# Kernel tuning notes

Hardware: AMD Instinct MI355X
Metric: run time of the kernel (lower is better)

The kernel has to match this reference:

```python
import jax, jax.numpy as jnp
import numpy as np

D_MODEL = 1024
D_FF = 4096
LN_EPS = 1e-5


def _layer_norm(x, gamma, beta):
    mu = jnp.mean(x, axis=-1, keepdims=True)
    var = jnp.mean(jnp.square(x - mu), axis=-1, keepdims=True)
    return (x - mu) * jax.lax.rsqrt(var + LN_EPS) * gamma + beta


def setup_inputs() -> dict:
    key = jax.random.key(0)
    ks = jax.random.split(key, 16)
    B, S, D, F = 2, 2048, D_MODEL, D_FF
    s_d = 1.0 / np.sqrt(D)
    s_f = 1.0 / np.sqrt(F)
    u = lambda k, shape, s: jax.random.uniform(k, shape, jnp.float32, -s, s)
    return {
        "x": jax.random.normal(ks[0], (B, S, D), jnp.float32),
        "wq": u(ks[1], (D, D), s_d), "bq": u(ks[2], (D,), s_d),
        "wk": u(ks[3], (D, D), s_d), "bk": u(ks[4], (D,), s_d),
        "wv": u(ks[5], (D, D), s_d), "bv": u(ks[6], (D,), s_d),
        "wo": u(ks[7], (D, D), s_d), "bo": u(ks[8], (D,), s_d),
        "w1": u(ks[9], (F, D), s_d), "b1": u(ks[10], (F,), s_d),
        "w2": u(ks[11], (D, F), s_f), "b2": u(ks[12], (D,), s_f),
        "g1": jnp.ones((D,), jnp.float32), "be1": jnp.zeros((D,), jnp.float32),
        "g2": jnp.ones((D,), jnp.float32), "be2": jnp.zeros((D,), jnp.float32),
        "num_heads": 16,
    }


def reference(x, wq, bq, wk, bk, wv, bv, wo, bo, w1, b1, w2, b2, g1, be1, g2, be2, num_heads):
    B, S, D = x.shape
    H = num_heads
    dk = D // H
    scale = 1.0 / np.sqrt(dk)

    # --- self-attention (pre-norm) ---
    h = _layer_norm(x, g1, be1)
    q = (h @ wq.T + bq).reshape(B, S, H, dk)
    k = (h @ wk.T + bk).reshape(B, S, H, dk)
    v = (h @ wv.T + bv).reshape(B, S, H, dk)
    scores = jnp.einsum("bqhd,bkhd->bhqk", q, k) * scale  # [B,H,S,S]
    attn = jax.nn.softmax(scores, axis=-1)
    ctx = jnp.einsum("bhqk,bkhd->bqhd", attn, v).reshape(B, S, D)
    x = x + ctx @ wo.T + bo

    # --- feed-forward (pre-norm, exact GELU as in torch default) ---
    h = _layer_norm(x, g2, be2)
    h = jax.nn.gelu(h @ w1.T + b1, approximate=False)
    x = x + h @ w2.T + b2
    return x
```

## Files before the change

### kernel.cpp

```cpp
#include <hip/hip_runtime.h>

typedef __attribute__((ext_vector_type(8))) __bf16 bf16x8;
typedef __attribute__((ext_vector_type(4))) __bf16 bf16x4;
typedef __attribute__((ext_vector_type(4))) float floatx4;
typedef void __attribute__((address_space(3))) lds_void_t;
typedef const void __attribute__((address_space(1))) gbl_void_t;

#define D_MODEL 1024
#define SEQ     2048
#define BATCH   2
#define NH      16
#define DK      64
#define DFF     4096
#define NTOK    (BATCH * SEQ)
#define QKVS    3072

#if __has_builtin(__builtin_amdgcn_exp2f)
#define EXP2(x) __builtin_amdgcn_exp2f(x)
#else
#define EXP2(x) exp2f(x)
#endif

__device__ __forceinline__ float gelu_exact(float x) {
    return 0.5f * x * (1.0f + erff(x * 0.70710678118654752f));
}

__global__ __launch_bounds__(256) void cast_all(const float* __restrict__ wq,
                                                const float* __restrict__ wk,
                                                const float* __restrict__ wv,
                                                const float* __restrict__ wo,
                                                const float* __restrict__ w1,
                                                const float* __restrict__ w2,
                                                __bf16* __restrict__ wqkvB,
                                                __bf16* __restrict__ woB,
                                                __bf16* __restrict__ w1B,
                                                __bf16* __restrict__ w2B) {
    int blk = blockIdx.x;
    const float* src;
    __bf16* dst;
    int base;
    const int NDD8 = (D_MODEL * D_MODEL) / 2048;
    if (blk < NDD8)          { src = wq; dst = wqkvB;                     base = blk; }
    else if (blk < 2 * NDD8) { src = wk; dst = wqkvB + D_MODEL * D_MODEL; base = blk - NDD8; }
    else if (blk < 3 * NDD8) { src = wv; dst = wqkvB + 2 * D_MODEL * D_MODEL; base = blk - 2 * NDD8; }
    else if (blk < 4 * NDD8) { src = wo; dst = woB;                       base = blk - 3 * NDD8; }
    else if (blk < 8 * NDD8) { src = w1; dst = w1B;                       base = blk - 4 * NDD8; }
    else                     { src = w2; dst = w2B;                       base = blk - 8 * NDD8; }
    int i = (base * 256 + threadIdx.x) * 8;
    floatx4 a = *(const floatx4*)(src + i);
    floatx4 b = *(const floatx4*)(src + i + 4);
    bf16x8 o;
    for (int j = 0; j < 4; ++j) { o[j] = (__bf16)a[j]; o[4 + j] = (__bf16)b[j]; }
    *(bf16x8*)(dst + i) = o;
}

__global__ __launch_bounds__(64) void ln_kernel(const float* __restrict__ x,
                                                const float* __restrict__ g,
                                                const float* __restrict__ b,
                                                __bf16* __restrict__ out) {
    int row = blockIdx.x, lane = threadIdx.x, base = lane * 16;
    const float* xr = x + (size_t)row * D_MODEL + base;
    float v[16];
    for (int j = 0; j < 4; ++j) {
        floatx4 a = *(const floatx4*)(xr + 4 * j);
        for (int i = 0; i < 4; ++i) v[4 * j + i] = a[i];
    }
    float s = 0.f, sq = 0.f;
    for (int i = 0; i < 16; ++i) { s += v[i]; sq += v[i] * v[i]; }
    for (int o = 1; o < 64; o <<= 1) { s += __shfl_xor(s, o); sq += __shfl_xor(sq, o); }
    float mu = s * (1.0f / D_MODEL);
    float var = sq * (1.0f / D_MODEL) - mu * mu;
    float rstd = rsqrtf(fmaxf(var, 0.f) + 1e-5f);

    const floatx4* gp = (const floatx4*)(g + base);
    const floatx4* bp = (const floatx4*)(b + base);
    bf16x8 o0, o1;
    for (int j = 0; j < 2; ++j) {
        floatx4 gv0 = gp[2 * j], gv1 = gp[2 * j + 1];
        floatx4 bv0 = bp[2 * j], bv1 = bp[2 * j + 1];
        for (int i = 0; i < 4; ++i) {
            float r0 = (v[8 * j + i] - mu) * rstd * gv0[i] + bv0[i];
            float r1 = (v[8 * j + 4 + i] - mu) * rstd * gv1[i] + bv1[i];
            if (j == 0) { o0[i] = (__bf16)r0; o0[4 + i] = (__bf16)r1; }
            else        { o1[i] = (__bf16)r0; o1[4 + i] = (__bf16)r1; }
        }
    }
    bf16x8* op = (bf16x8*)(out + (size_t)row * D_MODEL + base);
    op[0] = o0; op[1] = o1;
}

__global__ __launch_bounds__(64) void reduce_ln(const float* __restrict__ p0,
                                                const float* __restrict__ p1,
                                                const float* __restrict__ res,
                                                const float* __restrict__ bias,
                                                const float* __restrict__ g,
                                                const float* __restrict__ be,
                                                float* __restrict__ x1,
                                                __bf16* __restrict__ h2) {
    int row = blockIdx.x, lane = threadIdx.x, base = lane * 16;
    size_t off = (size_t)row * D_MODEL + base;
    float v[16];
    for (int j = 0; j < 4; ++j) {
        floatx4 a = *(const floatx4*)(p0 + off + 4 * j);
        floatx4 b = *(const floatx4*)(p1 + off + 4 * j);
        floatx4 r = *(const floatx4*)(res + off + 4 * j);
        floatx4 bv = *(const floatx4*)(bias + base + 4 * j);
        floatx4 o;
        for (int i = 0; i < 4; ++i) { o[i] = a[i] + b[i] + r[i] + bv[i]; v[4 * j + i] = o[i]; }
        *(floatx4*)(x1 + off + 4 * j) = o;
    }
    float s = 0.f, sq = 0.f;
    for (int i = 0; i < 16; ++i) { s += v[i]; sq += v[i] * v[i]; }
    for (int o = 1; o < 64; o <<= 1) { s += __shfl_xor(s, o); sq += __shfl_xor(sq, o); }
    float mu = s * (1.0f / D_MODEL);
    float var = sq * (1.0f / D_MODEL) - mu * mu;
    float rstd = rsqrtf(fmaxf(var, 0.f) + 1e-5f);

    const floatx4* gp = (const floatx4*)(g + base);
    const floatx4* bp = (const floatx4*)(be + base);
    bf16x8 o0, o1;
    for (int j = 0; j < 2; ++j) {
        floatx4 gv0 = gp[2 * j], gv1 = gp[2 * j + 1];
        floatx4 bv0 = bp[2 * j], bv1 = bp[2 * j + 1];
        for (int i = 0; i < 4; ++i) {
            float r0 = (v[8 * j + i] - mu) * rstd * gv0[i] + bv0[i];
            float r1 = (v[8 * j + 4 + i] - mu) * rstd * gv1[i] + bv1[i];
            if (j == 0) { o0[i] = (__bf16)r0; o0[4 + i] = (__bf16)r1; }
            else        { o1[i] = (__bf16)r0; o1[4 + i] = (__bf16)r1; }
        }
    }
    bf16x8* op = (bf16x8*)(h2 + off);
    op[0] = o0; op[1] = o1;
}

template <typename OutT, bool GELU, bool TRIBIAS, int KSPLIT>
__global__ __launch_bounds__(256) void gemm_bt(const __bf16* __restrict__ A,
                                               const __bf16* __restrict__ W,
                                               const float* __restrict__ bias0,
                                               const float* __restrict__ bias1,
                                               const float* __restrict__ bias2,
                                               const float* __restrict__ res,
                                               OutT* out, float* part1,
                                               int M, int N, int K) {
    __shared__ __bf16 AsF[2][4096];
    __shared__ __bf16 WsF[2][4096];

    int m0 = blockIdx.y * 128, n0 = blockIdx.x * 128;
    int t = threadIdx.x;
    int lane = t & 63, wave = t >> 6;
    int wm = (wave >> 1) * 64, wn = (wave & 1) * 64;
    int fr = lane & 15, quad = lane >> 4;
    int scol = quad * 8;

    int Ks = K / KSPLIT;
    int kbeg = (KSPLIT > 1) ? blockIdx.z * Ks : 0;

    floatx4 acc[4][4] = {};

    const __bf16* Abase = A + kbeg;
    const __bf16* Wbase = W + kbeg;

    auto stage = [&](int buf, int k0) {
#pragma unroll
        for (int p = 0; p < 2; ++p) {
            int blk = p * 4 + wave;
            int row = (blk >> 2) * 64 + (blk & 3) * 16 + fr;
            __builtin_amdgcn_global_load_lds(
                (gbl_void_t*)(Abase + (size_t)(m0 + row) * K + k0 + scol),
                (lds_void_t*)&AsF[buf][blk * 512], 16, 0, 0);
            __builtin_amdgcn_global_load_lds(
                (gbl_void_t*)(Wbase + (size_t)(n0 + row) * K + k0 + scol),
                (lds_void_t*)&WsF[buf][blk * 512], 16, 0, 0);
        }
    };

    auto compute = [&](int buf) {
        bf16x8 af[4], wf[4];
#pragma unroll
        for (int i = 0; i < 4; ++i)
            af[i] = *(const bf16x8*)&AsF[buf][((wave >> 1) * 4 + i) * 512 + lane * 8];
#pragma unroll
        for (int i = 0; i < 4; ++i)
            wf[i] = *(const bf16x8*)&WsF[buf][((wave & 1) * 4 + i) * 512 + lane * 8];
#pragma unroll
        for (int mi = 0; mi < 4; ++mi)
#pragma unroll
            for (int ni = 0; ni < 4; ++ni)
                acc[mi][ni] = __builtin_amdgcn_mfma_f32_16x16x32_bf16(wf[ni], af[mi], acc[mi][ni], 0, 0, 0);
    };

    int nsteps = Ks / 32;
    stage(0, 0);
    for (int s = 0; s < nsteps; ++s) {
        int cur = s & 1;
        __syncthreads();
        if (s + 1 < nsteps) stage(cur ^ 1, (s + 1) * 32);
        compute(cur);
    }

    if (KSPLIT > 1) {
        float* pb = (blockIdx.z == 0) ? (float*)out : part1;
#pragma unroll
        for (int mi = 0; mi < 4; ++mi) {
            int row = m0 + wm + mi * 16 + fr;
#pragma unroll
            for (int ni = 0; ni < 4; ++ni) {
                int col = n0 + wn + ni * 16 + quad * 4;
                *(floatx4*)(pb + (size_t)row * N + col) = acc[mi][ni];
            }
        }
    } else {
#pragma unroll
        for (int mi = 0; mi < 4; ++mi) {
            int row = m0 + wm + mi * 16 + fr;
#pragma unroll
            for (int ni = 0; ni < 4; ++ni) {
                int col = n0 + wn + ni * 16 + quad * 4;
                const float* bp = bias0;
                int bcol = col;
                if (TRIBIAS) { bp = col < 1024 ? bias0 : (col < 2048 ? bias1 : bias2); bcol = col & 1023; }
                floatx4 bv4 = *(const floatx4*)(bp + bcol);
                floatx4 v;
#pragma unroll
                for (int r = 0; r < 4; ++r) {
                    float x = acc[mi][ni][r] + bv4[r];
                    if (GELU) x = gelu_exact(x);
                    v[r] = x;
                }
                if (res) {
                    floatx4 r4 = *(const floatx4*)(res + (size_t)row * N + col);
#pragma unroll
                    for (int r = 0; r < 4; ++r) v[r] += r4[r];
                }
                if constexpr (sizeof(OutT) == 2) {
                    bf16x4 pk;
#pragma unroll
                    for (int r = 0; r < 4; ++r) pk[r] = (__bf16)v[r];
                    *(bf16x4*)((__bf16*)out + (size_t)row * N + col) = pk;
                } else {
                    *(floatx4*)((float*)out + (size_t)row * N + col) = v;
                }
            }
        }
    }
}

template <typename OutT, bool GELU, bool TRIBIAS>
__global__ __launch_bounds__(512) void gemm256(const __bf16* __restrict__ A,
                                               const __bf16* __restrict__ W,
                                               const float* __restrict__ bias0,
                                               const float* __restrict__ bias1,
                                               const float* __restrict__ bias2,
                                               OutT* out,
                                               int M, int N, int K) {
    __shared__ __bf16 AsF[2][8192];
    __shared__ __bf16 WsF[2][4096];

    int m0 = blockIdx.y * 256, n0 = blockIdx.x * 128;
    int t = threadIdx.x;
    int lane = t & 63, wave = t >> 6;
    int wm = (wave >> 1) * 64, wn = (wave & 1) * 64;
    int fr = lane & 15, quad = lane >> 4;
    int scol = quad * 8;

    floatx4 acc[4][4] = {};

    auto stage = [&](int buf, int k0) {
#pragma unroll
        for (int p = 0; p < 3; ++p) {
            int blk = wave * 3 + p;
            if (blk < 16) {
                int row = blk * 16 + fr;
                __builtin_amdgcn_global_load_lds(
                    (gbl_void_t*)(A + (size_t)(m0 + row) * K + k0 + scol),
                    (lds_void_t*)&AsF[buf][blk * 512], 16, 0, 0);
            } else {
                int row = (blk - 16) * 16 + fr;
                __builtin_amdgcn_global_load_lds(
                    (gbl_void_t*)(W + (size_t)(n0 + row) * K + k0 + scol),
                    (lds_void_t*)&WsF[buf][(blk - 16) * 512], 16, 0, 0);
            }
        }
    };

    auto compute = [&](int buf) {
        bf16x8 af[4], wf[4];
#pragma unroll
        for (int i = 0; i < 4; ++i)
            af[i] = *(const bf16x8*)&AsF[buf][((wave >> 1) * 4 + i) * 512 + lane * 8];
#pragma unroll
        for (int i = 0; i < 4; ++i)
            wf[i] = *(const bf16x8*)&WsF[buf][((wave & 1) * 4 + i) * 512 + lane * 8];
#pragma unroll
        for (int mi = 0; mi < 4; ++mi)
#pragma unroll
            for (int ni = 0; ni < 4; ++ni)
                acc[mi][ni] = __builtin_amdgcn_mfma_f32_16x16x32_bf16(wf[ni], af[mi], acc[mi][ni], 0, 0, 0);
    };

    int nsteps = K / 32;
    stage(0, 0);
    for (int s = 0; s < nsteps; ++s) {
        int cur = s & 1;
        __syncthreads();
        if (s + 1 < nsteps) stage(cur ^ 1, (s + 1) * 32);
        compute(cur);
    }

#pragma unroll
    for (int mi = 0; mi < 4; ++mi) {
        int row = m0 + wm + mi * 16 + fr;
#pragma unroll
        for (int ni = 0; ni < 4; ++ni) {
            int col = n0 + wn + ni * 16 + quad * 4;
            const float* bp = bias0;
            int bcol = col;
            if (TRIBIAS) { bp = col < 1024 ? bias0 : (col < 2048 ? bias1 : bias2); bcol = col & 1023; }
            floatx4 bv4 = *(const floatx4*)(bp + bcol);
            floatx4 v;
#pragma unroll
            for (int r = 0; r < 4; ++r) {
                float x = acc[mi][ni][r] + bv4[r];
                if (GELU) x = gelu_exact(x);
                v[r] = x;
            }
            if constexpr (sizeof(OutT) == 2) {
                bf16x4 pk;
#pragma unroll
                for (int r = 0; r < 4; ++r) pk[r] = (__bf16)v[r];
                *(bf16x4*)((__bf16*)out + (size_t)row * N + col) = pk;
            } else {
                *(floatx4*)((float*)out + (size_t)row * N + col) = v;
            }
        }
    }
}

__global__ __launch_bounds__(256) void reduce_k2(const float* __restrict__ p0,
                                                 const float* p1,
                                                 const float* __restrict__ res,
                                                 const float* __restrict__ bias,
                                                 float* out) {
    int i = (blockIdx.x * 256 + threadIdx.x) * 4;
    floatx4 a = *(const floatx4*)(p0 + i);
    floatx4 b = *(const floatx4*)(p1 + i);
    floatx4 r = *(const floatx4*)(res + i);
    floatx4 bv = *(const floatx4*)(bias + (i & 1023));
    floatx4 o;
#pragma unroll
    for (int j = 0; j < 4; ++j) o[j] = a[j] + b[j] + r[j] + bv[j];
    *(floatx4*)(out + i) = o;
}

__global__ __launch_bounds__(256) void transpose_v(const __bf16* __restrict__ qkv,
                                                   __bf16* __restrict__ vt) {
    __shared__ __bf16 tile[64][72];
    int b = blockIdx.z, h = blockIdx.y, s0 = blockIdx.x * 64;
    int t = threadIdx.x;
    int dl = (t & 7) * 8, sl = t >> 3;
    for (int p = 0; p < 2; ++p) {
        int s = sl + p * 32;
        bf16x8 val = *(const bf16x8*)(qkv + (size_t)(b * SEQ + s0 + s) * QKVS + 2048 + h * DK + dl);
        *(bf16x8*)&tile[s][dl] = val;
    }
    __syncthreads();
    int sl2 = (t & 7) * 8, d = t >> 3;
    for (int p = 0; p < 2; ++p) {
        int dd = d + p * 32;
        bf16x8 val;
        for (int j = 0; j < 8; ++j) val[j] = tile[sl2 + j][dd];
        *(bf16x8*)(vt + ((size_t)(b * NH + h) * DK + dd) * SEQ + s0 + sl2) = val;
    }
}

__global__ __launch_bounds__(256, 2) void attn_kernel(const __bf16* __restrict__ qkv,
                                                      const __bf16* __restrict__ vt,
                                                      __bf16* __restrict__ ctx) {
    __shared__ __bf16 Klds[8192];
    __shared__ __bf16 Vlds[8192];
    __shared__ __bf16 Plds[4][32][136];
    int b = blockIdx.z, h = blockIdx.y;
    int wave = threadIdx.x >> 6, lane = threadIdx.x & 63;
    int q0 = blockIdx.x * 128 + wave * 32;
    int fr = lane & 15, quad = lane >> 4;
    const float sc2 = 0.18033688011112042f;

    const __bf16* qp0 = qkv + (size_t)(b * SEQ + q0 + fr) * QKVS + h * DK + quad * 8;
    const __bf16* qp1 = qp0 + (size_t)16 * QKVS;
    bf16x8 qA0 = *(const bf16x8*)qp0, qB0 = *(const bf16x8*)(qp0 + 32);
    bf16x8 qA1 = *(const bf16x8*)qp1, qB1 = *(const bf16x8*)(qp1 + 32);

    const __bf16* kg = qkv + (size_t)b * SEQ * QKVS + 1024 + h * DK;
    const __bf16* vg = vt + (size_t)(b * NH + h) * DK * SEQ;

    floatx4 o[8] = {};
    float m0q = -1e30f, l0q = 0.f, m1q = -1e30f, l1q = 0.f;

    auto stage_tile = [&](int k0) {
#pragma unroll
        for (int p = 0; p < 4; ++p) {
            int bid = wave * 4 + p;
            int f = bid >> 1, half = bid & 1;
            __builtin_amdgcn_global_load_lds(
                (gbl_void_t*)(kg + (size_t)(k0 + f * 16 + fr) * QKVS + quad * 8 + half * 32),
                (lds_void_t*)&Klds[bid * 512], 16, 0, 0);
            int c = bid >> 2, ti = bid & 3;
            __builtin_amdgcn_global_load_lds(
                (gbl_void_t*)(vg + (size_t)(ti * 16 + fr) * SEQ + k0 + c * 32 + quad * 8),
                (lds_void_t*)&Vlds[bid * 512], 16, 0, 0);
        }
    };

    stage_tile(0);
    __syncthreads();

    for (int k0 = 0; k0 < SEQ; k0 += 128) {
        const __bf16* Kb = Klds + lane * 8;
        const __bf16* Vb = Vlds + lane * 8;
        bf16x8 kA[8], kB[8];
#pragma unroll
        for (int f = 0; f < 8; ++f) {
            kA[f] = *(const bf16x8*)(Kb + (f * 2 + 0) * 512);
            kB[f] = *(const bf16x8*)(Kb + (f * 2 + 1) * 512);
        }

        floatx4 s[8];
#pragma unroll
        for (int f = 0; f < 8; ++f) {
            floatx4 z = {0.f, 0.f, 0.f, 0.f};
            z = __builtin_amdgcn_mfma_f32_16x16x32_bf16(kA[f], qA0, z, 0, 0, 0);
            s[f] = __builtin_amdgcn_mfma_f32_16x16x32_bf16(kB[f], qB0, z, 0, 0, 0);
        }
        {
            float fm[8];
#pragma unroll
            for (int f = 0; f < 8; ++f)
                fm[f] = fmaxf(fmaxf(s[f][0], s[f][1]), fmaxf(s[f][2], s[f][3]));
            float mx = fmaxf(fmaxf(fmaxf(fm[0], fm[1]), fmaxf(fm[2], fm[3])),
                             fmaxf(fmaxf(fm[4], fm[5]), fmaxf(fm[6], fm[7])));
            float mx2 = mx * sc2;
            mx2 = fmaxf(mx2, __shfl_xor(mx2, 16));
            mx2 = fmaxf(mx2, __shfl_xor(mx2, 32));
            float mn = fmaxf(m0q, mx2);
            float alpha = EXP2(m0q - mn);
            m0q = mn;
            float r0 = 0.f, r1 = 0.f, r2 = 0.f, r3 = 0.f;
#pragma unroll
            for (int f = 0; f < 8; ++f) {
                bf16x4 pk;
                float p0 = EXP2(fmaf(s[f][0], sc2, -mn));
                float p1 = EXP2(fmaf(s[f][1], sc2, -mn));
                float p2 = EXP2(fmaf(s[f][2], sc2, -mn));
                float p3 = EXP2(fmaf(s[f][3], sc2, -mn));
                r0 += p0; r1 += p1; r2 += p2; r3 += p3;
                pk[0] = (__bf16)p0; pk[1] = (__bf16)p1; pk[2] = (__bf16)p2; pk[3] = (__bf16)p3;
                *(bf16x4*)&Plds[wave][fr][f * 16 + quad * 4] = pk;
            }
            float rs = (r0 + r1) + (r2 + r3);
            rs += __shfl_xor(rs, 16);
            rs += __shfl_xor(rs, 32);
            l0q = l0q * alpha + rs;
            float aB[4];
#pragma unroll
            for (int r = 0; r < 4; ++r) aB[r] = __shfl(alpha, quad * 4 + r);
#pragma unroll
            for (int ti = 0; ti < 4; ++ti)
#pragma unroll
                for (int r = 0; r < 4; ++r) o[ti][r] *= aB[r];
        }

        floatx4 s1[8];
#pragma unroll
        for (int f = 0; f < 8; ++f) {
            floatx4 z = {0.f, 0.f, 0.f, 0.f};
            z = __builtin_amdgcn_mfma_f32_16x16x32_bf16(kA[f], qA1, z, 0, 0, 0);
            s1[f] = __builtin_amdgcn_mfma_f32_16x16x32_bf16(kB[f], qB1, z, 0, 0, 0);
        }

        bf16x8 vf[4][4];
#pragma unroll
        for (int c = 0; c < 4; ++c)
#pragma unroll
            for (int ti = 0; ti < 4; ++ti)
                vf[c][ti] = *(const bf16x8*)(Vb + (c * 4 + ti) * 512);

        __syncthreads();
        if (k0 + 128 < SEQ) stage_tile(k0 + 128);

        {
            float fm[8];
#pragma unroll
            for (int f = 0; f < 8; ++f)
                fm[f] = fmaxf(fmaxf(s1[f][0], s1[f][1]), fmaxf(s1[f][2], s1[f][3]));
            float mx = fmaxf(fmaxf(fmaxf(fm[0], fm[1]), fmaxf(fm[2], fm[3])),
                             fmaxf(fmaxf(fm[4], fm[5]), fmaxf(fm[6], fm[7])));
            float mx2 = mx * sc2;
            mx2 = fmaxf(mx2, __shfl_xor(mx2, 16));
            mx2 = fmaxf(mx2, __shfl_xor(mx2, 32));
            float mn = fmaxf(m1q, mx2);
            float alpha = EXP2(m1q - mn);
            m1q = mn;
            float r0 = 0.f, r1 = 0.f, r2 = 0.f, r3 = 0.f;
#pragma unroll
            for (int f = 0; f < 8; ++f) {
                bf16x4 pk;
                float p0 = EXP2(fmaf(s1[f][0], sc2, -mn));
                float p1 = EXP2(fmaf(s1[f][1], sc2, -mn));
                float p2 = EXP2(fmaf(s1[f][2], sc2, -mn));
                float p3 = EXP2(fmaf(s1[f][3], sc2, -mn));
                r0 += p0; r1 += p1; r2 += p2; r3 += p3;
                pk[0] = (__bf16)p0; pk[1] = (__bf16)p1; pk[2] = (__bf16)p2; pk[3] = (__bf16)p3;
                *(bf16x4*)&Plds[wave][16 + fr][f * 16 + quad * 4] = pk;
            }
            float rs = (r0 + r1) + (r2 + r3);
            rs += __shfl_xor(rs, 16);
            rs += __shfl_xor(rs, 32);
            l1q = l1q * alpha + rs;
            float aB[4];
#pragma unroll
            for (int r = 0; r < 4; ++r) aB[r] = __shfl(alpha, quad * 4 + r);
#pragma unroll
            for (int ti = 0; ti < 4; ++ti)
#pragma unroll
                for (int r = 0; r < 4; ++r) o[4 + ti][r] *= aB[r];
        }
        __threadfence_block();

        bf16x8 pa0[4], pa1[4];
#pragma unroll
        for (int c = 0; c < 4; ++c) {
            pa0[c] = *(const bf16x8*)&Plds[wave][fr][c * 32 + quad * 8];
            pa1[c] = *(const bf16x8*)&Plds[wave][16 + fr][c * 32 + quad * 8];
        }
#pragma unroll
        for (int c = 0; c < 4; ++c)
#pragma unroll
            for (int ti = 0; ti < 4; ++ti) {
                o[ti]     = __builtin_amdgcn_mfma_f32_16x16x32_bf16(pa0[c], vf[c][ti], o[ti], 0, 0, 0);
                o[4 + ti] = __builtin_amdgcn_mfma_f32_16x16x32_bf16(pa1[c], vf[c][ti], o[4 + ti], 0, 0, 0);
            }
        __threadfence_block();

        __syncthreads();
    }
    float lB0[4], lB1[4];
#pragma unroll
    for (int r = 0; r < 4; ++r) {
        lB0[r] = __shfl(l0q, quad * 4 + r);
        lB1[r] = __shfl(l1q, quad * 4 + r);
    }
#pragma unroll
    for (int ti = 0; ti < 4; ++ti)
#pragma unroll
        for (int r = 0; r < 4; ++r) {
            ctx[(size_t)(b * SEQ + q0 + quad * 4 + r) * D_MODEL + h * DK + ti * 16 + fr] =
                (__bf16)(o[ti][r] / lB0[r]);
            ctx[(size_t)(b * SEQ + q0 + 16 + quad * 4 + r) * D_MODEL + h * DK + ti * 16 + fr] =
                (__bf16)(o[4 + ti][r] / lB1[r]);
        }
}

extern "C" void kernel_launch(void* const* d_in, const int* in_sizes, int n_in,
                              void* d_out, int out_size, void* d_ws, size_t ws_size,
                              hipStream_t stream) {
    const float* x   = (const float*)d_in[0];
    const float* wq  = (const float*)d_in[1];
    const float* bq  = (const float*)d_in[2];
    const float* wk  = (const float*)d_in[3];
    const float* bk  = (const float*)d_in[4];
    const float* wv  = (const float*)d_in[5];
    const float* bv  = (const float*)d_in[6];
    const float* wo  = (const float*)d_in[7];
    const float* bo  = (const float*)d_in[8];
    const float* w1  = (const float*)d_in[9];
    const float* b1  = (const float*)d_in[10];
    const float* w2  = (const float*)d_in[11];
    const float* b2  = (const float*)d_in[12];
    const float* g1  = (const float*)d_in[13];
    const float* be1 = (const float*)d_in[14];
    const float* g2  = (const float*)d_in[15];
    const float* be2 = (const float*)d_in[16];
    float* out = (float*)d_out;

    char* ws = (char*)d_ws;
    const size_t MB = 1024 * 1024;
    __bf16* wqkvB = (__bf16*)(ws);
    __bf16* woB   = (__bf16*)(ws + 6 * MB);
    __bf16* w1B   = (__bf16*)(ws + 8 * MB);
    __bf16* w2B   = (__bf16*)(ws + 16 * MB);
    __bf16* h1    = (__bf16*)(ws + 24 * MB);
    float*  x1    = (float*)(ws + 24 * MB);
    __bf16* qkv   = (__bf16*)(ws + 40 * MB);
    __bf16* vt    = (__bf16*)(ws + 64 * MB);
    __bf16* ffh   = (__bf16*)(ws + 40 * MB);
    float*  pA0   = (float*)(ws + 40 * MB);
    float*  pA1   = (float*)(ws + 56 * MB);
    float*  pF0   = (float*)(ws);
    __bf16* ctx   = (__bf16*)d_out;
    __bf16* h2    = (__bf16*)d_out;

    dim3 gQKV(QKVS / 128, NTOK / 256);
    dim3 gDz(D_MODEL / 128, NTOK / 128, 2);
    dim3 gF(DFF / 128, NTOK / 256);
    dim3 gTr(SEQ / 64, NH, BATCH);
    dim3 gAttn(SEQ / 128, NH, BATCH);
    int gRed = NTOK * D_MODEL / (256 * 4);

    cast_all<<<6144, 256, 0, stream>>>(wq, wk, wv, wo, w1, w2, wqkvB, woB, w1B, w2B);
    ln_kernel<<<NTOK, 64, 0, stream>>>(x, g1, be1, h1);
    gemm256<__bf16, false, true><<<gQKV, 512, 0, stream>>>(h1, wqkvB, bq, bk, bv, qkv, NTOK, QKVS, D_MODEL);
    transpose_v<<<gTr, 256, 0, stream>>>(qkv, vt);
    attn_kernel<<<gAttn, 256, 0, stream>>>(qkv, vt, ctx);
    gemm_bt<float, false, false, 2><<<gDz, 256, 0, stream>>>(ctx, woB, nullptr, nullptr, nullptr, nullptr, pA0, pA1, NTOK, D_MODEL, D_MODEL);
    reduce_ln<<<NTOK, 64, 0, stream>>>(pA0, pA1, x, bo, g2, be2, x1, h2);
    gemm256<__bf16, true, false><<<gF, 512, 0, stream>>>(h2, w1B, b1, b1, b1, ffh, NTOK, DFF, D_MODEL);
    gemm_bt<float, false, false, 2><<<gDz, 256, 0, stream>>>(ffh, w2B, nullptr, nullptr, nullptr, nullptr, pF0, (float*)d_out, NTOK, D_MODEL, DFF);
    reduce_k2<<<gRed, 256, 0, stream>>>(pF0, (float*)d_out, x1, b2, out);
}
```

Baseline: 433.9 us.

## Replace 256x128 GEMM with 256x256 eight-phase pipelined kernel for QKV and FFN1

Rewrites the QKV and FFN-up GEMM as a 256x256 tile kernel with K-step 64. Each K-tile is split into phases that interleave async global-to-LDS loads of the next A/B halves with MFMA work. It uses explicit vmcnt waits, raw barriers, s_setprio around the MFMA bursts, and reuses W fragments across M halves. The aim is more data reuse per tile and better overlap of memory and compute. In exchange it takes 128KB of LDS, more accumulator registers, and fewer blocks in the grid (e.g. 192 for QKV), which may underfill the CUs.

```diff
diff --git a/kernel.cpp b/kernel.cpp
--- a/kernel.cpp
+++ b/kernel.cpp
@@ -246,73 +246,111 @@
 }
 
 template <typename OutT, bool GELU, bool TRIBIAS>
-__global__ __launch_bounds__(512) void gemm256(const __bf16* __restrict__ A,
-                                               const __bf16* __restrict__ W,
-                                               const float* __restrict__ bias0,
-                                               const float* __restrict__ bias1,
-                                               const float* __restrict__ bias2,
-                                               OutT* out,
-                                               int M, int N, int K) {
-    __shared__ __bf16 AsF[2][8192];
-    __shared__ __bf16 WsF[2][4096];
-
-    int m0 = blockIdx.y * 256, n0 = blockIdx.x * 128;
-    int t = threadIdx.x;
-    int lane = t & 63, wave = t >> 6;
-    int wm = (wave >> 1) * 64, wn = (wave & 1) * 64;
+__global__ __launch_bounds__(512, 2) void gemm8p(const __bf16* __restrict__ A,
+                                                 const __bf16* __restrict__ W,
+                                                 const float* __restrict__ bias0,
+                                                 const float* __restrict__ bias1,
+                                                 const float* __restrict__ bias2,
+                                                 OutT* out,
+                                                 int M, int N, int K) {
+    __shared__ __bf16 AsF[2][16384];
+    __shared__ __bf16 WsF[2][16384];
+
+    int m0 = blockIdx.y * 256, n0 = blockIdx.x * 256;
+    int lane = threadIdx.x & 63, wave = threadIdx.x >> 6;
+    int wr = wave >> 2, wc = wave & 3;
     int fr = lane & 15, quad = lane >> 4;
     int scol = quad * 8;
 
-    floatx4 acc[4][4] = {};
-
-    auto stage = [&](int buf, int k0) {
-#pragma unroll
-        for (int p = 0; p < 3; ++p) {
-            int blk = wave * 3 + p;
-            if (blk < 16) {
-                int row = blk * 16 + fr;
-                __builtin_amdgcn_global_load_lds(
-                    (gbl_void_t*)(A + (size_t)(m0 + row) * K + k0 + scol),
-                    (lds_void_t*)&AsF[buf][blk * 512], 16, 0, 0);
-            } else {
-                int row = (blk - 16) * 16 + fr;
-                __builtin_amdgcn_global_load_lds(
-                    (gbl_void_t*)(W + (size_t)(n0 + row) * K + k0 + scol),
-                    (lds_void_t*)&WsF[buf][(blk - 16) * 512], 16, 0, 0);
-            }
+    floatx4 acc[8][4] = {};
+
+    auto stageA = [&](int t, int h) {
+        int buf = t & 1, k0 = t * 64;
+#pragma unroll
+        for (int j = 0; j < 2; ++j) {
+            int blk = h * 16 + wave * 2 + j;
+            int row = (blk >> 1) * 16 + fr, col = k0 + (blk & 1) * 32 + scol;
+            __builtin_amdgcn_global_load_lds(
+                (gbl_void_t*)(A + (size_t)(m0 + row) * K + col),
+                (lds_void_t*)&AsF[buf][blk * 512], 16, 0, 0);
         }
     };
-
-    auto compute = [&](int buf) {
-        bf16x8 af[4], wf[4];
-#pragma unroll
-        for (int i = 0; i < 4; ++i)
-            af[i] = *(const bf16x8*)&AsF[buf][((wave >> 1) * 4 + i) * 512 + lane * 8];
-#pragma unroll
-        for (int i = 0; i < 4; ++i)
-            wf[i] = *(const bf16x8*)&WsF[buf][((wave & 1) * 4 + i) * 512 + lane * 8];
-#pragma unroll
-        for (int mi = 0; mi < 4; ++mi)
+    auto stageB = [&](int t, int h) {
+        int buf = t & 1, k0 = t * 64;
+#pragma unroll
+        for (int j = 0; j < 2; ++j) {
+            int blk = h * 16 + wave * 2 + j;
+            int row = (blk >> 1) * 16 + fr, col = k0 + (blk & 1) * 32 + scol;
+            __builtin_amdgcn_global_load_lds(
+                (gbl_void_t*)(W + (size_t)(n0 + row) * K + col),
+                (lds_void_t*)&WsF[buf][blk * 512], 16, 0, 0);
+        }
+    };
+
+    bf16x8 wf0[4], wf1[4];
+    auto phase = [&](int buf, int mh, int kh, bf16x8* wfX, bool readwf) {
+        bf16x8 af[4];
+#pragma unroll
+        for (int j = 0; j < 4; ++j)
+            af[j] = *(const bf16x8*)&AsF[buf][((wr * 8 + mh * 4 + j) * 2 + kh) * 512 + lane * 8];
+        if (readwf) {
 #pragma unroll
             for (int ni = 0; ni < 4; ++ni)
-                acc[mi][ni] = __builtin_amdgcn_mfma_f32_16x16x32_bf16(wf[ni], af[mi], acc[mi][ni], 0, 0, 0);
+                wfX[ni] = *(const bf16x8*)&WsF[buf][((wc * 4 + ni) * 2 + kh) * 512 + lane * 8];
+        }
+        __builtin_amdgcn_s_setprio(1);
+#pragma unroll
+        for (int j = 0; j < 4; ++j)
+#pragma unroll
+            for (int ni = 0; ni < 4; ++ni)
+                acc[mh * 4 + j][ni] =
+                    __builtin_amdgcn_mfma_f32_16x16x32_bf16(wfX[ni], af[j], acc[mh * 4 + j][ni], 0, 0, 0);
+        __builtin_amdgcn_s_setprio(0);
     };
 
-    int nsteps = K / 32;
-    stage(0, 0);
-    for (int s = 0; s < nsteps; ++s) {
-        int cur = s & 1;
-        __syncthreads();
-        if (s + 1 < nsteps) stage(cur ^ 1, (s + 1) * 32);
-        compute(cur);
-    }
-
-#pragma unroll
-    for (int mi = 0; mi < 4; ++mi) {
-        int row = m0 + wm + mi * 16 + fr;
+#define PH_BAR() do { __builtin_amdgcn_s_barrier(); __builtin_amdgcn_sched_barrier(0); } while (0)
+
+    int ntiles = K / 64, niter = ntiles / 2;
+    stageB(0, 0); stageB(0, 1); stageA(0, 0); stageA(0, 1); stageB(1, 0); stageB(1, 1);
+    for (int i = 0; i < niter; ++i) {
+        int t1 = 2 * i + 1;
+        bool nolast = (i + 1 < niter);
+        asm volatile("s_waitcnt vmcnt(4)" ::: "memory");
+        PH_BAR();
+        stageA(t1, 0);
+        phase(0, 0, 0, wf0, true);
+        PH_BAR();
+        stageA(t1, 1);
+        phase(0, 0, 1, wf1, true);
+        PH_BAR();
+        if (nolast) stageB(t1 + 1, 0);
+        phase(0, 1, 0, wf0, false);
+        PH_BAR();
+        if (nolast) stageB(t1 + 1, 1);
+        phase(0, 1, 1, wf1, false);
+        if (nolast) { asm volatile("s_waitcnt vmcnt(4)" ::: "memory"); }
+        else        { asm volatile("s_waitcnt vmcnt(0)" ::: "memory"); }
+        PH_BAR();
+        if (nolast) stageA(t1 + 1, 0);
+        phase(1, 0, 0, wf0, true);
+        PH_BAR();
+        if (nolast) stageA(t1 + 1, 1);
+        phase(1, 0, 1, wf1, true);
+        PH_BAR();
+        if (nolast) stageB(t1 + 2, 0);
+        phase(1, 1, 0, wf0, false);
+        PH_BAR();
+        if (nolast) stageB(t1 + 2, 1);
+        phase(1, 1, 1, wf1, false);
+    }
+#undef PH_BAR
+
+#pragma unroll
+    for (int mi = 0; mi < 8; ++mi) {
+        int row = m0 + wr * 128 + mi * 16 + fr;
 #pragma unroll
         for (int ni = 0; ni < 4; ++ni) {
-            int col = n0 + wn + ni * 16 + quad * 4;
+            int col = n0 + wc * 64 + ni * 16 + quad * 4;
             const float* bp = bias0;
             int bcol = col;
             if (TRIBIAS) { bp = col < 1024 ? bias0 : (col < 2048 ? bias1 : bias2); bcol = col & 1023; }
@@ -599,21 +637,21 @@
     __bf16* ctx   = (__bf16*)d_out;
     __bf16* h2    = (__bf16*)d_out;
 
-    dim3 gQKV(QKVS / 128, NTOK / 256);
+    dim3 gQKV(QKVS / 256, NTOK / 256);
     dim3 gDz(D_MODEL / 128, NTOK / 128, 2);
-    dim3 gF(DFF / 128, NTOK / 256);
+    dim3 gF(DFF / 256, NTOK / 256);
     dim3 gTr(SEQ / 64, NH, BATCH);
     dim3 gAttn(SEQ / 128, NH, BATCH);
     int gRed = NTOK * D_MODEL / (256 * 4);
 
     cast_all<<<6144, 256, 0, stream>>>(wq, wk, wv, wo, w1, w2, wqkvB, woB, w1B, w2B);
     ln_kernel<<<NTOK, 64, 0, stream>>>(x, g1, be1, h1);
-    gemm256<__bf16, false, true><<<gQKV, 512, 0, stream>>>(h1, wqkvB, bq, bk, bv, qkv, NTOK, QKVS, D_MODEL);
+    gemm8p<__bf16, false, true><<<gQKV, 512, 0, stream>>>(h1, wqkvB, bq, bk, bv, qkv, NTOK, QKVS, D_MODEL);
     transpose_v<<<gTr, 256, 0, stream>>>(qkv, vt);
     attn_kernel<<<gAttn, 256, 0, stream>>>(qkv, vt, ctx);
     gemm_bt<float, false, false, 2><<<gDz, 256, 0, stream>>>(ctx, woB, nullptr, nullptr, nullptr, nullptr, pA0, pA1, NTOK, D_MODEL, D_MODEL);
     reduce_ln<<<NTOK, 64, 0, stream>>>(pA0, pA1, x, bo, g2, be2, x1, h2);
-    gemm256<__bf16, true, false><<<gF, 512, 0, stream>>>(h2, w1B, b1, b1, b1, ffh, NTOK, DFF, D_MODEL);
+    gemm8p<__bf16, true, false><<<gF, 512, 0, stream>>>(h2, w1B, b1, b1, b1, ffh, NTOK, DFF, D_MODEL);
     gemm_bt<float, false, false, 2><<<gDz, 256, 0, stream>>>(ffh, w2B, nullptr, nullptr, nullptr, nullptr, pF0, (float*)d_out, NTOK, D_MODEL, DFF);
     reduce_k2<<<gRed, 256, 0, stream>>>(pF0, (float*)d_out, x1, b2, out);
 }
```

Measured after the change: 431.6 us. About the same (-0.5%).
